# Kernel optimization log

Measured on AMD Instinct MI355X. Metric: run time of the kernel, lower is better.

## Reference

```python
import jax, jax.numpy as jnp
import numpy as np

D = 256; HEADS = 8; DH = D // HEADS; LEVELS = 4; POINTS = 4; NLAYERS = 6; DFF = 1024
SHAPES = ((92, 160), (46, 80), (23, 40), (12, 20))  # (H, W) per level
LEN = sum(h * w for h, w in SHAPES)  # 19560
BS = 4; NQ = 900; EPS = 1e-5
SCALE = 1.0 / float(np.sqrt(DH))


def setup_inputs() -> dict:
    ks = iter(jax.random.split(jax.random.key(0), 64))
    def rn(shape, s=0.02):
        return jax.random.normal(next(ks), shape, jnp.float32) * s
    inp = {}
    inp['tgt'] = jax.random.normal(next(ks), (BS, NQ, D), jnp.float32)
    inp['reference_points'] = jax.random.uniform(next(ks), (BS, NQ, 3), jnp.float32)
    inp['src'] = jax.random.normal(next(ks), (BS, LEN, D), jnp.float32)
    inp['valid_ratios'] = jnp.ones((BS, LEVELS, 2), jnp.float32)
    inp['query_pos'] = jax.random.normal(next(ks), (BS, NQ, D), jnp.float32)
    # per-layer stacked parameters [NLAYERS, ...]
    inp['sa_in_w'] = rn((NLAYERS, 3 * D, D)); inp['sa_in_b'] = jnp.zeros((NLAYERS, 3 * D))
    inp['sa_out_w'] = rn((NLAYERS, D, D)); inp['sa_out_b'] = jnp.zeros((NLAYERS, D))
    inp['samp_w'] = rn((NLAYERS, HEADS * LEVELS * POINTS * 2, D), 0.01)
    inp['samp_b'] = jax.random.uniform(next(ks), (NLAYERS, HEADS * LEVELS * POINTS * 2), jnp.float32, -2.0, 2.0)
    inp['attn_w'] = rn((NLAYERS, HEADS * LEVELS * POINTS, D)); inp['attn_b'] = jnp.zeros((NLAYERS, HEADS * LEVELS * POINTS))
    inp['val_w'] = rn((NLAYERS, D, D)); inp['val_b'] = jnp.zeros((NLAYERS, D))
    inp['ca_out_w'] = rn((NLAYERS, D, D)); inp['ca_out_b'] = jnp.zeros((NLAYERS, D))
    inp['ffn1_w'] = rn((NLAYERS, DFF, D)); inp['ffn1_b'] = jnp.zeros((NLAYERS, DFF))
    inp['ffn2_w'] = rn((NLAYERS, D, DFF)); inp['ffn2_b'] = jnp.zeros((NLAYERS, D))
    for i in (1, 2, 3):
        inp['ln%d_w' % i] = jnp.ones((NLAYERS, D)); inp['ln%d_b' % i] = jnp.zeros((NLAYERS, D))
    return inp


def _ln(x, w, b):
    mu = x.mean(-1, keepdims=True)
    var = ((x - mu) ** 2).mean(-1, keepdims=True)
    return (x - mu) / jnp.sqrt(var + EPS) * w + b


def _self_attn(q, k, v, in_w, in_b, out_w, out_b):
    wq, wk, wv = jnp.split(in_w, 3, 0)
    bq, bk, bv = jnp.split(in_b, 3, 0)
    def proj(x, w, b):
        return (x @ w.T + b).reshape(BS, -1, HEADS, DH).transpose(0, 2, 1, 3)
    qh, kh, vh = proj(q, wq, bq), proj(k, wk, bk), proj(v, wv, bv)
    att = jax.nn.softmax(jnp.einsum('bhqd,bhkd->bhqk', qh * SCALE, kh), axis=-1)
    o = jnp.einsum('bhqk,bhkd->bhqd', att, vh).transpose(0, 2, 1, 3).reshape(BS, -1, D)
    return o @ out_w.T + out_b


def _msda(query, ref, src, sw, sb, aw, ab, vw, vb, ow, ob):
    # query [bs,NQ,D]; ref [bs,NQ,LEVELS,2] normalized xz coords
    value = (src @ vw.T + vb).reshape(BS, LEN, HEADS, DH)
    off = (query @ sw.T + sb).reshape(BS, NQ, HEADS, LEVELS, POINTS, 2)
    attn = jax.nn.softmax((query @ aw.T + ab).reshape(BS, NQ, HEADS, LEVELS * POINTS), -1)
    attn = attn.reshape(BS, NQ, HEADS, LEVELS, POINTS)
    norm = jnp.asarray([[w, h] for h, w in SHAPES], jnp.float32)  # (W,H) per level
    loc = ref[:, :, None, :, None, :] + off / norm[None, None, None, :, None, :]
    out = jnp.zeros((BS, HEADS, NQ, DH), jnp.float32)
    start = 0
    for l, (H, W) in enumerate(SHAPES):
        v_l = value[:, start:start + H * W].transpose(0, 2, 1, 3)  # [bs,heads,HW,dh]
        start += H * W
        ll = loc[:, :, :, l]  # [bs,NQ,heads,P,2]
        x = ll[..., 0] * W - 0.5
        y = ll[..., 1] * H - 0.5
        x0 = jnp.floor(x); y0 = jnp.floor(y)
        fx = x - x0; fy = y - y0
        x0i = x0.astype(jnp.int32); y0i = y0.astype(jnp.int32)
        def gather(xi, yi):
            inb = ((xi >= 0) & (xi < W) & (yi >= 0) & (yi < H)).astype(jnp.float32)
            idx = jnp.clip(yi, 0, H - 1) * W + jnp.clip(xi, 0, W - 1)
            idxt = idx.transpose(0, 2, 1, 3).reshape(BS, HEADS, NQ * POINTS, 1)
            g = jnp.take_along_axis(v_l, idxt, axis=2).reshape(BS, HEADS, NQ, POINTS, DH)
            return g * inb.transpose(0, 2, 1, 3)[..., None]
        def wt(w4):
            return w4.transpose(0, 2, 1, 3)[..., None]
        samp = (gather(x0i, y0i) * wt((1 - fx) * (1 - fy))
                + gather(x0i + 1, y0i) * wt(fx * (1 - fy))
                + gather(x0i, y0i + 1) * wt((1 - fx) * fy)
                + gather(x0i + 1, y0i + 1) * wt(fx * fy))
        out = out + (samp * attn[:, :, :, l].transpose(0, 2, 1, 3)[..., None]).sum(3)
    out = out.transpose(0, 2, 1, 3).reshape(BS, NQ, D)
    return out @ ow.T + ob


def _forward(tgt, reference_points, src, valid_ratios, query_pos,
             sa_in_w, sa_in_b, sa_out_w, sa_out_b,
             samp_w, samp_b, attn_w, attn_b, val_w, val_b, ca_out_w, ca_out_b,
             ffn1_w, ffn1_b, ffn2_w, ffn2_b,
             ln1_w, ln1_b, ln2_w, ln2_b, ln3_w, ln3_b):
    # reference_points last dim == 3 (x,y,z); deformable attn uses (x,z)
    ref_xz = jnp.concatenate([reference_points[..., :1], reference_points[..., 2:]], -1)
    ref_in = ref_xz[:, :, None] * valid_ratios[:, None]  # [bs,NQ,LEVELS,2]
    out = tgt
    for l in range(NLAYERS):
        q = out + query_pos
        sa = _self_attn(q, q, out, sa_in_w[l], sa_in_b[l], sa_out_w[l], sa_out_b[l])
        out = _ln(out + sa, ln1_w[l], ln1_b[l])
        ca = _msda(out + query_pos, ref_in, src, samp_w[l], samp_b[l], attn_w[l], attn_b[l],
                   val_w[l], val_b[l], ca_out_w[l], ca_out_b[l])
        out = _ln(out + ca, ln2_w[l], ln2_b[l])
        h = jax.nn.relu(out @ ffn1_w[l].T + ffn1_b[l]) @ ffn2_w[l].T + ffn2_b[l]
        out = _ln(out + h, ln3_w[l], ln3_b[l])
    return out


def reference(tgt, reference_points, src, valid_ratios, query_pos,
              sa_in_w, sa_in_b, sa_out_w, sa_out_b,
              samp_w, samp_b, attn_w, attn_b, val_w, val_b, ca_out_w, ca_out_b,
              ffn1_w, ffn1_b, ffn2_w, ffn2_b,
              ln1_w, ln1_b, ln2_w, ln2_b, ln3_w, ln3_b):
    return _forward(tgt, reference_points, src, valid_ratios, query_pos,
                    sa_in_w, sa_in_b, sa_out_w, sa_out_b,
                    samp_w, samp_b, attn_w, attn_b, val_w, val_b, ca_out_w, ca_out_b,
                    ffn1_w, ffn1_b, ffn2_w, ffn2_b,
                    ln1_w, ln1_b, ln2_w, ln2_b, ln3_w, ln3_b)
```

## Files before the change

### kernel.cpp

```cpp
#include <hip/hip_runtime.h>
#include <math.h>

#define DMODEL 256
#define HEADS 8
#define DHEAD 32
#define LEVELS 4
#define POINTS 4
#define NLAYERS 6
#define DFF 1024
#define BS 4
#define NQ 900
#define SLEN 19560
#define EPS_LN 1e-5f
#define ATT_SCALE 0.17677669529663689f

typedef __attribute__((ext_vector_type(8))) short bf16x8;
typedef __attribute__((ext_vector_type(4))) float f32x4;
typedef __attribute__((ext_vector_type(4))) unsigned short u16x4;
typedef __attribute__((ext_vector_type(8))) unsigned short u16x8;

__device__ __forceinline__ unsigned short f2b(float x) {
  unsigned u = __float_as_uint(x);
  u += 0x7FFF + ((u >> 16) & 1);
  return (unsigned short)(u >> 16);
}
__device__ __forceinline__ float b2f(unsigned short v) {
  return __uint_as_float(((unsigned)v) << 16);
}

__global__ __launch_bounds__(256) void copycvt_k(const float* __restrict__ a,
                                                 const float* __restrict__ qp,
                                                 float* __restrict__ cf,
                                                 unsigned short* __restrict__ cb,
                                                 unsigned short* __restrict__ qb, int n4) {
  int i = blockIdx.x * 256 + threadIdx.x;
  if (i < n4) {
    float4 v = reinterpret_cast<const float4*>(a)[i];
    float4 q = reinterpret_cast<const float4*>(qp)[i];
    reinterpret_cast<float4*>(cf)[i] = v;
    u16x4 o4 = {f2b(v.x), f2b(v.y), f2b(v.z), f2b(v.w)};
    reinterpret_cast<u16x4*>(cb)[i] = o4;
    u16x4 p4 = {f2b(v.x + q.x), f2b(v.y + q.y), f2b(v.z + q.z), f2b(v.w + q.w)};
    reinterpret_cast<u16x4*>(qb)[i] = p4;
  }
}

#define N4_SRC (SLEN * BS * DMODEL / 4)
#define N4_SAIN (NLAYERS * 768 * 256 / 4)
#define N4_SQ (NLAYERS * 256 * 256 / 4)
#define N4_FFN (NLAYERS * DFF * 256 / 4)
__global__ __launch_bounds__(256) void f2ball_k(
    const float* __restrict__ s0, const float* __restrict__ s1,
    const float* __restrict__ s2, const float* __restrict__ s3,
    const float* __restrict__ s4, const float* __restrict__ s5,
    const float* __restrict__ s6,
    unsigned short* __restrict__ d0, unsigned short* __restrict__ d1,
    unsigned short* __restrict__ d2, unsigned short* __restrict__ d3,
    unsigned short* __restrict__ d4, unsigned short* __restrict__ d5,
    unsigned short* __restrict__ d6) {
  const int total = N4_SRC + N4_SAIN + 3 * N4_SQ + 2 * N4_FFN;
  for (int i = blockIdx.x * 256 + threadIdx.x; i < total; i += gridDim.x * 256) {
    const float* s;
    unsigned short* d;
    int j = i;
    if (j < N4_SRC) { s = s0; d = d0; }
    else { j -= N4_SRC;
      if (j < N4_SAIN) { s = s1; d = d1; }
      else { j -= N4_SAIN;
        if (j < N4_SQ) { s = s2; d = d2; }
        else { j -= N4_SQ;
          if (j < N4_SQ) { s = s3; d = d3; }
          else { j -= N4_SQ;
            if (j < N4_SQ) { s = s4; d = d4; }
            else { j -= N4_SQ;
              if (j < N4_FFN) { s = s5; d = d5; }
              else { j -= N4_FFN; s = s6; d = d6; } } } } } }
    float4 v = reinterpret_cast<const float4*>(s)[j];
    u16x4 o4 = {f2b(v.x), f2b(v.y), f2b(v.z), f2b(v.w)};
    reinterpret_cast<u16x4*>(d)[j] = o4;
  }
}

__global__ __launch_bounds__(256) void catw_k(const float* __restrict__ sw,
                                              const float* __restrict__ aw,
                                              const float* __restrict__ sb,
                                              const float* __restrict__ ab,
                                              unsigned short* __restrict__ wout,
                                              float* __restrict__ bout) {
  int i = blockIdx.x * 256 + threadIdx.x;
  const int total4 = NLAYERS * 384 * 256 / 4;
  if (i < total4) {
    int l = i / (384 * 64);
    int r = i % (384 * 64);
    int row = r / 64;
    int c4 = r % 64;
    const float* srcp = row < 256
        ? sw + ((size_t)l * 256 * 256 + (size_t)row * 256 + c4 * 4)
        : aw + ((size_t)l * 128 * 256 + (size_t)(row - 256) * 256 + c4 * 4);
    float4 v = *(const float4*)srcp;
    u16x4 o4 = {f2b(v.x), f2b(v.y), f2b(v.z), f2b(v.w)};
    *(u16x4*)(wout + (size_t)i * 4) = o4;
  }
  if (i < NLAYERS * 384) {
    int l = i / 384, r = i % 384;
    bout[i] = r < 256 ? sb[l * 256 + r] : ab[l * 128 + (r - 256)];
  }
}

__global__ __launch_bounds__(256) void gemm_bf_k(const unsigned short* __restrict__ A,
                                                 const unsigned short* __restrict__ W,
                                                 const float* __restrict__ bias,
                                                 const float* __restrict__ res,
                                                 float* __restrict__ outf,
                                                 unsigned short* __restrict__ outb,
                                                 int ldo, int M, int N, int K, int relu) {
  __shared__ unsigned short As[64][72];
  __shared__ unsigned short Ws[64][72];
  const int tid = threadIdx.x;
  const int lane = tid & 63, wv = tid >> 6;
  const int wm = wv >> 1, wn = wv & 1;
  const int m0 = blockIdx.x * 64, n0 = blockIdx.y * 64;
  const int l15 = lane & 15, l4 = lane >> 4;

  f32x4 acc[2][2] = {};
  for (int k0 = 0; k0 < K; k0 += 64) {
#pragma unroll
    for (int t = 0; t < 2; ++t) {
      int u = t * 256 + tid;
      int r = u >> 3, c8 = u & 7;
      int ra = m0 + r; if (ra >= M) ra = M - 1;
      *(u16x8*)&As[r][c8 * 8] = *(const u16x8*)(A + (size_t)ra * K + k0 + c8 * 8);
      *(u16x8*)&Ws[r][c8 * 8] = *(const u16x8*)(W + (size_t)(n0 + r) * K + k0 + c8 * 8);
    }
    __syncthreads();
#pragma unroll
    for (int ks = 0; ks < 64; ks += 32) {
      bf16x8 af[2], wf[2];
#pragma unroll
      for (int fr = 0; fr < 2; ++fr)
        af[fr] = *(const bf16x8*)&As[wm * 32 + fr * 16 + l15][ks + l4 * 8];
#pragma unroll
      for (int fn = 0; fn < 2; ++fn)
        wf[fn] = *(const bf16x8*)&Ws[wn * 32 + fn * 16 + l15][ks + l4 * 8];
#pragma unroll
      for (int fr = 0; fr < 2; ++fr)
#pragma unroll
        for (int fn = 0; fn < 2; ++fn)
          acc[fr][fn] = __builtin_amdgcn_mfma_f32_16x16x32_bf16(
              af[fr], wf[fn], acc[fr][fn], 0, 0, 0);
    }
    __syncthreads();
  }
#pragma unroll
  for (int fr = 0; fr < 2; ++fr)
#pragma unroll
    for (int fn = 0; fn < 2; ++fn) {
      int col = n0 + wn * 32 + fn * 16 + l15;
      float bs = bias[col];
#pragma unroll
      for (int j = 0; j < 4; ++j) {
        int row = m0 + wm * 32 + fr * 16 + l4 * 4 + j;
        if (row >= M) continue;
        float v = acc[fr][fn][j] + bs;
        if (res) v += res[(size_t)row * ldo + col];
        if (relu) v = fmaxf(v, 0.f);
        if (outf) outf[(size_t)row * ldo + col] = v;
        if (outb) outb[(size_t)row * ldo + col] = f2b(v);
      }
    }
}

__global__ __launch_bounds__(256) void gemm_vmfma_k(const unsigned short* __restrict__ A,
                                                    const unsigned short* __restrict__ W,
                                                    const float* __restrict__ bias,
                                                    unsigned short* __restrict__ C,
                                                    int M) {
  __shared__ unsigned short As[128][72];
  __shared__ unsigned short Ws[128][72];
  const int tid = threadIdx.x;
  const int lane = tid & 63, wv = tid >> 6;
  const int wm = wv >> 1, wn = wv & 1;
  const int m0 = blockIdx.x * 128, n0 = blockIdx.y * 128;
  const int l15 = lane & 15, l4 = lane >> 4;

  f32x4 acc[4][4] = {};

  for (int k0 = 0; k0 < 256; k0 += 64) {
#pragma unroll
    for (int t = 0; t < 4; ++t) {
      int u = t * 256 + tid;
      int r = u >> 3, c8 = u & 7;
      int ra = m0 + r; if (ra >= M) ra = M - 1;
      *(u16x8*)&As[r][c8 * 8] = *(const u16x8*)(A + (size_t)ra * 256 + k0 + c8 * 8);
      *(u16x8*)&Ws[r][c8 * 8] = *(const u16x8*)(W + (size_t)(n0 + r) * 256 + k0 + c8 * 8);
    }
    __syncthreads();
#pragma unroll
    for (int ks = 0; ks < 64; ks += 32) {
      bf16x8 af[4], bf[4];
#pragma unroll
      for (int fr = 0; fr < 4; ++fr)
        af[fr] = *(const bf16x8*)&As[wm * 64 + fr * 16 + l15][ks + l4 * 8];
#pragma unroll
      for (int fn = 0; fn < 4; ++fn)
        bf[fn] = *(const bf16x8*)&Ws[wn * 64 + fn * 16 + l15][ks + l4 * 8];
#pragma unroll
      for (int fr = 0; fr < 4; ++fr)
#pragma unroll
        for (int fn = 0; fn < 4; ++fn)
          acc[fr][fn] = __builtin_amdgcn_mfma_f32_16x16x32_bf16(
              af[fr], bf[fn], acc[fr][fn], 0, 0, 0);
    }
    __syncthreads();
  }
#pragma unroll
  for (int fr = 0; fr < 4; ++fr)
#pragma unroll
    for (int fn = 0; fn < 4; ++fn) {
      int col = n0 + wn * 64 + fn * 16 + l15;
      float bs = bias[col];
#pragma unroll
      for (int j = 0; j < 4; ++j) {
        int row = m0 + wm * 64 + fr * 16 + l4 * 4 + j;
        if (row < M) C[(size_t)row * 256 + col] = f2b(acc[fr][fn][j] + bs);
      }
    }
}

__global__ __launch_bounds__(256) void fattn_mfma_k(const unsigned short* __restrict__ qkv,
                                                    unsigned short* __restrict__ o) {
  __shared__ unsigned short Qlds[64][40];
  __shared__ unsigned short Klds[64][40];
  __shared__ unsigned short Vt[32][72];
  __shared__ unsigned short Plds[64][72];
  const int tid = threadIdx.x;
  const int lane = tid & 63;
  const int wq = tid >> 6;
  const int l15 = lane & 15, l4 = lane >> 4;
  const int q0 = blockIdx.x * 64;
  const int h = blockIdx.y, b = blockIdx.z;
  const int hq = h * 32;
  const size_t rowb = (size_t)b * NQ;

  {
    int q = q0 + (tid >> 2);
    int qc = q < NQ ? q : NQ - 1;
    *(u16x8*)&Qlds[tid >> 2][(tid & 3) * 8] =
        *(const u16x8*)(qkv + (rowb + qc) * 768 + hq + (tid & 3) * 8);
  }
  __syncthreads();
  const bf16x8 qf = *(const bf16x8*)&Qlds[wq * 16 + l15][l4 * 8];

  float m_r[4] = {-1e30f, -1e30f, -1e30f, -1e30f};
  float l_r[4] = {0.f, 0.f, 0.f, 0.f};
  f32x4 oacc[2] = {};

  for (int k0 = 0; k0 < NQ; k0 += 64) {
    __syncthreads();
    {
      int kk = k0 + (tid >> 2);
      int kc = kk < NQ ? kk : NQ - 1;
      const unsigned short* kbase = qkv + (rowb + kc) * 768 + hq + (tid & 3) * 8;
      u16x8 kv = *(const u16x8*)(kbase + 256);
      u16x8 vv = *(const u16x8*)(kbase + 512);
      *(u16x8*)&Klds[tid >> 2][(tid & 3) * 8] = kv;
#pragma unroll
      for (int i = 0; i < 8; ++i) Vt[(tid & 3) * 8 + i][tid >> 2] = vv[i];
    }
    __syncthreads();

    f32x4 s[4];
#pragma unroll
    for (int fc = 0; fc < 4; ++fc) {
      bf16x8 kf = *(const bf16x8*)&Klds[fc * 16 + l15][l4 * 8];
      s[fc] = __builtin_amdgcn_mfma_f32_16x16x32_bf16(qf, kf, (f32x4){0.f, 0.f, 0.f, 0.f}, 0, 0, 0);
    }
#pragma unroll
    for (int fc = 0; fc < 4; ++fc) {
      bool oob = (k0 + fc * 16 + l15) >= NQ;
#pragma unroll
      for (int j = 0; j < 4; ++j)
        s[fc][j] = oob ? -1e30f : s[fc][j] * ATT_SCALE;
    }
#pragma unroll
    for (int j = 0; j < 4; ++j) {
      float tm = fmaxf(fmaxf(s[0][j], s[1][j]), fmaxf(s[2][j], s[3][j]));
      tm = fmaxf(tm, __shfl_xor(tm, 1, 16));
      tm = fmaxf(tm, __shfl_xor(tm, 2, 16));
      tm = fmaxf(tm, __shfl_xor(tm, 4, 16));
      tm = fmaxf(tm, __shfl_xor(tm, 8, 16));
      float mn = fmaxf(m_r[j], tm);
      float sf = __expf(m_r[j] - mn);
      m_r[j] = mn;
      oacc[0][j] *= sf;
      oacc[1][j] *= sf;
      float rs = 0.f;
#pragma unroll
      for (int fc = 0; fc < 4; ++fc) {
        float pv = __expf(s[fc][j] - mn);
        s[fc][j] = pv;
        rs += pv;
      }
      rs += __shfl_xor(rs, 1, 16);
      rs += __shfl_xor(rs, 2, 16);
      rs += __shfl_xor(rs, 4, 16);
      rs += __shfl_xor(rs, 8, 16);
      l_r[j] = l_r[j] * sf + rs;
    }
#pragma unroll
    for (int fc = 0; fc < 4; ++fc)
#pragma unroll
      for (int j = 0; j < 4; ++j)
        Plds[wq * 16 + l4 * 4 + j][fc * 16 + l15] = f2b(s[fc][j]);
    __syncthreads();
#pragma unroll
    for (int ks = 0; ks < 2; ++ks) {
      bf16x8 pf = *(const bf16x8*)&Plds[wq * 16 + l15][ks * 32 + l4 * 8];
#pragma unroll
      for (int oc = 0; oc < 2; ++oc) {
        bf16x8 vf = *(const bf16x8*)&Vt[oc * 16 + l15][ks * 32 + l4 * 8];
        oacc[oc] = __builtin_amdgcn_mfma_f32_16x16x32_bf16(pf, vf, oacc[oc], 0, 0, 0);
      }
    }
  }
#pragma unroll
  for (int j = 0; j < 4; ++j) {
    int q = q0 + wq * 16 + l4 * 4 + j;
    if (q < NQ) {
      float inv = 1.f / l_r[j];
      o[(rowb + q) * 256 + hq + l15] = f2b(oacc[0][j] * inv);
      o[(rowb + q) * 256 + hq + 16 + l15] = f2b(oacc[1][j] * inv);
    }
  }
}

__global__ __launch_bounds__(256) void msda_k(const float* __restrict__ refp,
                                              const float* __restrict__ vr,
                                              const unsigned short* __restrict__ value,
                                              const float* __restrict__ cat,
                                              unsigned short* __restrict__ outp) {
  const int HW[4][2] = {{92, 160}, {46, 80}, {23, 40}, {12, 20}};
  const int START[4] = {0, 14720, 18400, 19320};
  const int qi = blockIdx.x, b = blockIdx.y;
  const int tid = threadIdx.x;
  const int h = tid >> 5;
  const int r = tid & 31;
  const int lvl = r >> 3;
  const int li = r & 7;
  const size_t base = (size_t)(b * NQ + qi);
  const float rx = refp[base * 3 + 0];
  const float rz = refp[base * 3 + 2];

  const float* lg = cat + base * 384 + 256 + h * 16;
  float4 L0 = *(const float4*)(lg + 0);
  float4 L1 = *(const float4*)(lg + 4);
  float4 L2 = *(const float4*)(lg + 8);
  float4 L3 = *(const float4*)(lg + 12);
  float mx = fmaxf(fmaxf(fmaxf(L0.x, L0.y), fmaxf(L0.z, L0.w)),
                   fmaxf(fmaxf(fmaxf(L1.x, L1.y), fmaxf(L1.z, L1.w)),
                         fmaxf(fmaxf(fmaxf(L2.x, L2.y), fmaxf(L2.z, L2.w)),
                               fmaxf(fmaxf(L3.x, L3.y), fmaxf(L3.z, L3.w)))));
  float4 E0 = {__expf(L0.x - mx), __expf(L0.y - mx), __expf(L0.z - mx), __expf(L0.w - mx)};
  float4 E1 = {__expf(L1.x - mx), __expf(L1.y - mx), __expf(L1.z - mx), __expf(L1.w - mx)};
  float4 E2 = {__expf(L2.x - mx), __expf(L2.y - mx), __expf(L2.z - mx), __expf(L2.w - mx)};
  float4 E3 = {__expf(L3.x - mx), __expf(L3.y - mx), __expf(L3.z - mx), __expf(L3.w - mx)};
  float sum = E0.x + E0.y + E0.z + E0.w + E1.x + E1.y + E1.z + E1.w +
              E2.x + E2.y + E2.z + E2.w + E3.x + E3.y + E3.z + E3.w;
  const float inv = 1.f / sum;
  float4 Emy = lvl == 0 ? E0 : lvl == 1 ? E1 : lvl == 2 ? E2 : E3;
  float wl[4] = {Emy.x * inv, Emy.y * inv, Emy.z * inv, Emy.w * inv};

  const int H = HW[lvl][0], W = HW[lvl][1];
  const float refx = rx * vr[(b * LEVELS + lvl) * 2 + 0] * (float)W;
  const float refy = rz * vr[(b * LEVELS + lvl) * 2 + 1] * (float)H;
  const unsigned short* vbase = value + ((size_t)b * SLEN + START[lvl]) * DMODEL + h * DHEAD + li * 4;
  const float* ob = cat + base * 384 + h * 32 + lvl * 8;

  float a0 = 0.f, a1 = 0.f, a2 = 0.f, a3 = 0.f;
#pragma unroll
  for (int p = 0; p < 4; ++p) {
    const float x = refx + ob[p * 2 + 0] - 0.5f;
    const float y = refy + ob[p * 2 + 1] - 0.5f;
    const float x0f = floorf(x), y0f = floorf(y);
    const float fx = x - x0f, fy = y - y0f;
    const int x0 = (int)x0f, y0 = (int)y0f;
#pragma unroll
    for (int ci = 0; ci < 4; ++ci) {
      const int xi = x0 + (ci & 1);
      const int yi = y0 + (ci >> 1);
      if ((xi >= 0) && (xi < W) && (yi >= 0) && (yi < H)) {
        const float wxy = ((ci & 1) ? fx : 1.f - fx) * ((ci >> 1) ? fy : 1.f - fy) * wl[p];
        u16x4 v4 = *(const u16x4*)(vbase + (size_t)(yi * W + xi) * DMODEL);
        a0 = fmaf(wxy, b2f(v4[0]), a0);
        a1 = fmaf(wxy, b2f(v4[1]), a1);
        a2 = fmaf(wxy, b2f(v4[2]), a2);
        a3 = fmaf(wxy, b2f(v4[3]), a3);
      }
    }
  }
  a0 += __shfl_xor(a0, 8);  a1 += __shfl_xor(a1, 8);
  a2 += __shfl_xor(a2, 8);  a3 += __shfl_xor(a3, 8);
  a0 += __shfl_xor(a0, 16); a1 += __shfl_xor(a1, 16);
  a2 += __shfl_xor(a2, 16); a3 += __shfl_xor(a3, 16);
  if (lvl == 0) {
    u16x4 o4 = {f2b(a0), f2b(a1), f2b(a2), f2b(a3)};
    *(u16x4*)(outp + base * 256 + h * 32 + li * 4) = o4;
  }
}

__global__ __launch_bounds__(256) void ln_k(const float* __restrict__ src,
                                            const float* __restrict__ w,
                                            const float* __restrict__ bias,
                                            const float* __restrict__ qpos,
                                            float* __restrict__ dst,
                                            unsigned short* __restrict__ dstb,
                                            unsigned short* __restrict__ qposb) {
  const int row = blockIdx.x * 4 + (threadIdx.x >> 6);
  const int lane = threadIdx.x & 63;
  const size_t o = (size_t)row * DMODEL + lane * 4;
  float4 x = *(const float4*)(src + o);
  float s = x.x + x.y + x.z + x.w;
#pragma unroll
  for (int m = 1; m < 64; m <<= 1) s += __shfl_xor(s, m);
  const float mu = s * (1.f / DMODEL);
  float4 v = {x.x - mu, x.y - mu, x.z - mu, x.w - mu};
  float q = v.x * v.x + v.y * v.y + v.z * v.z + v.w * v.w;
#pragma unroll
  for (int m = 1; m < 64; m <<= 1) q += __shfl_xor(q, m);
  const float rstd = rsqrtf(q * (1.f / DMODEL) + EPS_LN);
  float4 wv = *(const float4*)(w + lane * 4);
  float4 bv = *(const float4*)(bias + lane * 4);
  float4 y = {v.x * rstd * wv.x + bv.x, v.y * rstd * wv.y + bv.y,
              v.z * rstd * wv.z + bv.z, v.w * rstd * wv.w + bv.w};
  *(float4*)(dst + o) = y;
  if (dstb) {
    u16x4 ob = {f2b(y.x), f2b(y.y), f2b(y.z), f2b(y.w)};
    *(u16x4*)(dstb + o) = ob;
  }
  if (qposb) {
    float4 qv = *(const float4*)(qpos + o);
    u16x4 ob = {f2b(y.x + qv.x), f2b(y.y + qv.y), f2b(y.z + qv.z), f2b(y.w + qv.w)};
    *(u16x4*)(qposb + o) = ob;
  }
}

extern "C" void kernel_launch(void* const* d_in, const int* in_sizes, int n_in,
                              void* d_out, int out_size, void* d_ws, size_t ws_size,
                              hipStream_t stream) {
  const float* tgt     = (const float*)d_in[0];
  const float* refp    = (const float*)d_in[1];
  const float* src     = (const float*)d_in[2];
  const float* vr      = (const float*)d_in[3];
  const float* qpos    = (const float*)d_in[4];
  const float* sa_in_w = (const float*)d_in[5];
  const float* sa_in_b = (const float*)d_in[6];
  const float* sa_out_w= (const float*)d_in[7];
  const float* sa_out_b= (const float*)d_in[8];
  const float* samp_w  = (const float*)d_in[9];
  const float* samp_b  = (const float*)d_in[10];
  const float* attn_w  = (const float*)d_in[11];
  const float* attn_b  = (const float*)d_in[12];
  const float* val_w   = (const float*)d_in[13];
  const float* val_b   = (const float*)d_in[14];
  const float* ca_out_w= (const float*)d_in[15];
  const float* ca_out_b= (const float*)d_in[16];
  const float* ffn1_w  = (const float*)d_in[17];
  const float* ffn1_b  = (const float*)d_in[18];
  const float* ffn2_w  = (const float*)d_in[19];
  const float* ffn2_b  = (const float*)d_in[20];
  const float* ln1_w   = (const float*)d_in[21];
  const float* ln1_b   = (const float*)d_in[22];
  const float* ln2_w   = (const float*)d_in[23];
  const float* ln2_b   = (const float*)d_in[24];
  const float* ln3_w   = (const float*)d_in[25];
  const float* ln3_b   = (const float*)d_in[26];

  const int M = BS * NQ;
  const int MV = BS * SLEN;
  const size_t TOK = (size_t)M * DMODEL;

  float* ws = (float*)d_ws;
  size_t off = 0;
  auto alloc = [&](size_t n) { float* p = ws + off; off += n; return p; };
  auto allocb = [&](size_t n) { unsigned short* p = (unsigned short*)(ws + off); off += (n + 1) / 2; return p; };
  float* cur    = alloc(TOK);
  float* tmp    = alloc(TOK);
  float* catout = alloc((size_t)M * 384);
  float* b_cacat= alloc((size_t)NLAYERS * 384);
  unsigned short* cur_bf  = allocb(TOK);
  unsigned short* qbuf_bf = allocb(TOK);
  unsigned short* sao_bf  = allocb(TOK);
  unsigned short* msda_bf = allocb(TOK);
  unsigned short* qkv_bf  = allocb((size_t)M * 768);
  unsigned short* ffnh_bf = allocb((size_t)M * DFF);
  unsigned short* src_bf  = allocb((size_t)MV * DMODEL);
  unsigned short* value_bf= allocb((size_t)MV * DMODEL);
  unsigned short* w_in_bf   = allocb((size_t)NLAYERS * 768 * 256);
  unsigned short* w_saout_bf= allocb((size_t)NLAYERS * 256 * 256);
  unsigned short* w_cacat_bf= allocb((size_t)NLAYERS * 384 * 256);
  unsigned short* w_val_bf  = allocb((size_t)NLAYERS * 256 * 256);
  unsigned short* w_caout_bf= allocb((size_t)NLAYERS * 256 * 256);
  unsigned short* w_ffn1_bf = allocb((size_t)NLAYERS * DFF * 256);
  unsigned short* w_ffn2_bf = allocb((size_t)NLAYERS * 256 * DFF);

  const int n4 = (int)(TOK / 4);
  const dim3 blk(256);
  const dim3 gE((n4 + 255) / 256);

  copycvt_k<<<gE, blk, 0, stream>>>(tgt, qpos, cur, cur_bf, qbuf_bf, n4);
  f2ball_k<<<dim3(2048), blk, 0, stream>>>(src, sa_in_w, sa_out_w, val_w, ca_out_w,
                                           ffn1_w, ffn2_w,
                                           src_bf, w_in_bf, w_saout_bf, w_val_bf,
                                           w_caout_bf, w_ffn1_bf, w_ffn2_bf);
  catw_k<<<dim3(576), blk, 0, stream>>>(samp_w, attn_w, samp_b, attn_b, w_cacat_bf, b_cacat);

  const dim3 gQK((M + 63) / 64, 512 / 64);
  const dim3 gV((M + 63) / 64, 256 / 64);
  const dim3 gN256((M + 63) / 64, 256 / 64);
  const dim3 gCat((M + 63) / 64, 384 / 64);
  const dim3 gF1((M + 63) / 64, DFF / 64);
  const dim3 gLN(M / 4);

  for (int l = 0; l < NLAYERS; ++l) {
    const unsigned short* wq = w_in_bf + (size_t)l * 768 * 256;
    const float* bq = sa_in_b + (size_t)l * 768;

    gemm_bf_k<<<gQK, blk, 0, stream>>>(qbuf_bf, wq, bq, nullptr,
                                       nullptr, qkv_bf, 768, M, 512, 256, 0);
    gemm_bf_k<<<gV, blk, 0, stream>>>(cur_bf, wq + 512 * 256, bq + 512, nullptr,
                                      nullptr, qkv_bf + 512, 768, M, 256, 256, 0);

    fattn_mfma_k<<<dim3((NQ + 63) / 64, HEADS, BS), blk, 0, stream>>>(qkv_bf, sao_bf);

    gemm_bf_k<<<gN256, blk, 0, stream>>>(sao_bf, w_saout_bf + (size_t)l * 256 * 256,
                                         sa_out_b + l * 256, cur, tmp, nullptr, 256, M, 256, 256, 0);
    ln_k<<<gLN, blk, 0, stream>>>(tmp, ln1_w + l * 256, ln1_b + l * 256, qpos,
                                  cur, nullptr, qbuf_bf);

    gemm_vmfma_k<<<dim3((MV + 127) / 128, 2), blk, 0, stream>>>(
        src_bf, w_val_bf + (size_t)l * 256 * 256, val_b + l * 256, value_bf, MV);
    gemm_bf_k<<<gCat, blk, 0, stream>>>(qbuf_bf, w_cacat_bf + (size_t)l * 384 * 256,
                                        b_cacat + l * 384, nullptr, catout, nullptr, 384, M, 384, 256, 0);

    msda_k<<<dim3(NQ, BS), blk, 0, stream>>>(refp, vr, value_bf, catout, msda_bf);

    gemm_bf_k<<<gN256, blk, 0, stream>>>(msda_bf, w_caout_bf + (size_t)l * 256 * 256,
                                         ca_out_b + l * 256, cur, tmp, nullptr, 256, M, 256, 256, 0);
    ln_k<<<gLN, blk, 0, stream>>>(tmp, ln2_w + l * 256, ln2_b + l * 256, nullptr,
                                  cur, cur_bf, nullptr);

    gemm_bf_k<<<gF1, blk, 0, stream>>>(cur_bf, w_ffn1_bf + (size_t)l * DFF * 256,
                                       ffn1_b + l * DFF, nullptr, nullptr, ffnh_bf, DFF, M, DFF, 256, 1);
    gemm_bf_k<<<gN256, blk, 0, stream>>>(ffnh_bf, w_ffn2_bf + (size_t)l * 256 * DFF,
                                         ffn2_b + l * 256, cur, tmp, nullptr, 256, M, 256, DFF, 0);
    const bool last = (l == NLAYERS - 1);
    ln_k<<<gLN, blk, 0, stream>>>(tmp, ln3_w + l * 256, ln3_b + l * 256,
                                  last ? nullptr : qpos,
                                  last ? (float*)d_out : cur,
                                  last ? nullptr : cur_bf,
                                  last ? nullptr : qbuf_bf);
  }
}
```

Measured before the change: 1.399 ms.

## Fuse residual+LayerNorm into GEMM epilogue and precompute query_pos projections

Adds a full-row GEMM kernel (32 rows x 256 cols per block) that applies bias, residual and LayerNorm in its epilogue, replacing the separate GEMM + ln_k pairs and the tmp buffer. Uses linearity to precompute query_pos projections for the Q/K and sampling/attention weights of all layers once up front. Per-layer GEMMs then take cur_bf as input and add the precomputed qpos term as a residual instead of bias, which also merges the QK and V projections into one launch. This trades extra workspace and one large upfront GEMM for fewer launches and fewer round trips through memory. The wide-N fused kernel has lower block-level parallelism and reloads the full 256-row weight tile per block.

```diff
diff --git a/kernel.cpp b/kernel.cpp
--- a/kernel.cpp
+++ b/kernel.cpp
@@ -40,7 +40,7 @@
     reinterpret_cast<float4*>(cf)[i] = v;
     u16x4 o4 = {f2b(v.x), f2b(v.y), f2b(v.z), f2b(v.w)};
     reinterpret_cast<u16x4*>(cb)[i] = o4;
-    u16x4 p4 = {f2b(v.x + q.x), f2b(v.y + q.y), f2b(v.z + q.z), f2b(v.w + q.w)};
+    u16x4 p4 = {f2b(q.x), f2b(q.y), f2b(q.z), f2b(q.w)};
     reinterpret_cast<u16x4*>(qb)[i] = p4;
   }
 }
@@ -107,10 +107,31 @@
   }
 }
 
+__global__ __launch_bounds__(256) void stackqk_k(const float* __restrict__ w_in,
+                                                 const float* __restrict__ b_in,
+                                                 unsigned short* __restrict__ qkW,
+                                                 float* __restrict__ bqk) {
+  int i = blockIdx.x * 256 + threadIdx.x;
+  const int total4 = NLAYERS * 512 * 256 / 4;
+  if (i < total4) {
+    int l = i / (512 * 64);
+    int r = i % (512 * 64);
+    int row = r / 64, c4 = r % 64;
+    float4 v = *(const float4*)(w_in + (size_t)l * 768 * 256 + (size_t)row * 256 + c4 * 4);
+    u16x4 o4 = {f2b(v.x), f2b(v.y), f2b(v.z), f2b(v.w)};
+    *(u16x4*)(qkW + ((size_t)(l * 512 + row) * 256 + c4 * 4)) = o4;
+  }
+  if (i < NLAYERS * 512) {
+    int l = i / 512, r = i % 512;
+    bqk[i] = b_in[l * 768 + r];
+  }
+}
+
 __global__ __launch_bounds__(256) void gemm_bf_k(const unsigned short* __restrict__ A,
                                                  const unsigned short* __restrict__ W,
                                                  const float* __restrict__ bias,
                                                  const float* __restrict__ res,
+                                                 int res_n, int ldr,
                                                  float* __restrict__ outf,
                                                  unsigned short* __restrict__ outb,
                                                  int ldo, int M, int N, int K, int relu) {
@@ -161,13 +182,106 @@
       for (int j = 0; j < 4; ++j) {
         int row = m0 + wm * 32 + fr * 16 + l4 * 4 + j;
         if (row >= M) continue;
-        float v = acc[fr][fn][j] + bs;
-        if (res) v += res[(size_t)row * ldo + col];
+        float v = acc[fr][fn][j];
+        if (res && col < res_n) v += res[(size_t)row * ldr + col];
+        else v += bs;
         if (relu) v = fmaxf(v, 0.f);
         if (outf) outf[(size_t)row * ldo + col] = v;
         if (outb) outb[(size_t)row * ldo + col] = f2b(v);
       }
     }
+}
+
+__global__ __launch_bounds__(256) void gemm_lnres_k(const unsigned short* __restrict__ A,
+                                                    const unsigned short* __restrict__ W,
+                                                    const float* __restrict__ bias,
+                                                    const float* __restrict__ res,
+                                                    const float* __restrict__ lnw,
+                                                    const float* __restrict__ lnb,
+                                                    float* __restrict__ outf,
+                                                    unsigned short* __restrict__ outb,
+                                                    int M, int K) {
+  __shared__ unsigned short As[32][72];
+  __shared__ unsigned short Ws[256][72];
+  __shared__ float Os[32][264];
+  const int tid = threadIdx.x;
+  const int lane = tid & 63, wv = tid >> 6;
+  const int l15 = lane & 15, l4 = lane >> 4;
+  const int m0 = blockIdx.x * 32;
+
+  f32x4 acc[2][4] = {};
+  for (int k0 = 0; k0 < K; k0 += 64) {
+    {
+      int r = tid >> 3, c8 = tid & 7;
+      int ra = m0 + r; if (ra >= M) ra = M - 1;
+      *(u16x8*)&As[r][c8 * 8] = *(const u16x8*)(A + (size_t)ra * K + k0 + c8 * 8);
+#pragma unroll
+      for (int t = 0; t < 8; ++t) {
+        int u = t * 256 + tid;
+        int wr = u >> 3, wc = u & 7;
+        *(u16x8*)&Ws[wr][wc * 8] = *(const u16x8*)(W + (size_t)wr * K + k0 + wc * 8);
+      }
+    }
+    __syncthreads();
+#pragma unroll
+    for (int ks = 0; ks < 64; ks += 32) {
+      bf16x8 af[2], wf[4];
+#pragma unroll
+      for (int fr = 0; fr < 2; ++fr)
+        af[fr] = *(const bf16x8*)&As[fr * 16 + l15][ks + l4 * 8];
+#pragma unroll
+      for (int fc = 0; fc < 4; ++fc)
+        wf[fc] = *(const bf16x8*)&Ws[wv * 64 + fc * 16 + l15][ks + l4 * 8];
+#pragma unroll
+      for (int fr = 0; fr < 2; ++fr)
+#pragma unroll
+        for (int fc = 0; fc < 4; ++fc)
+          acc[fr][fc] = __builtin_amdgcn_mfma_f32_16x16x32_bf16(
+              af[fr], wf[fc], acc[fr][fc], 0, 0, 0);
+    }
+    __syncthreads();
+  }
+#pragma unroll
+  for (int fr = 0; fr < 2; ++fr)
+#pragma unroll
+    for (int fc = 0; fc < 4; ++fc) {
+      int col = wv * 64 + fc * 16 + l15;
+      float bs = bias[col];
+#pragma unroll
+      for (int j = 0; j < 4; ++j) {
+        int row = fr * 16 + l4 * 4 + j;
+        int grow = m0 + row;
+        float v = acc[fr][fc][j] + bs + (grow < M ? res[(size_t)grow * 256 + col] : 0.f);
+        Os[row][col] = v;
+      }
+    }
+  __syncthreads();
+  float4 wv4 = *(const float4*)(lnw + lane * 4);
+  float4 bv4 = *(const float4*)(lnb + lane * 4);
+#pragma unroll
+  for (int i = 0; i < 8; ++i) {
+    int row = wv * 8 + i;
+    int grow = m0 + row;
+    float4 x = *(float4*)&Os[row][lane * 4];
+    float s = x.x + x.y + x.z + x.w;
+#pragma unroll
+    for (int m = 1; m < 64; m <<= 1) s += __shfl_xor(s, m);
+    const float mu = s * (1.f / DMODEL);
+    float4 v = {x.x - mu, x.y - mu, x.z - mu, x.w - mu};
+    float q = v.x * v.x + v.y * v.y + v.z * v.z + v.w * v.w;
+#pragma unroll
+    for (int m = 1; m < 64; m <<= 1) q += __shfl_xor(q, m);
+    const float rstd = rsqrtf(q * (1.f / DMODEL) + EPS_LN);
+    float4 y = {v.x * rstd * wv4.x + bv4.x, v.y * rstd * wv4.y + bv4.y,
+                v.z * rstd * wv4.z + bv4.z, v.w * rstd * wv4.w + bv4.w};
+    if (grow < M) {
+      *(float4*)(outf + (size_t)grow * 256 + lane * 4) = y;
+      if (outb) {
+        u16x4 ob = {f2b(y.x), f2b(y.y), f2b(y.z), f2b(y.w)};
+        *(u16x4*)(outb + (size_t)grow * 256 + lane * 4) = ob;
+      }
+    }
+  }
 }
 
 __global__ __launch_bounds__(256) void gemm_vmfma_k(const unsigned short* __restrict__ A,
@@ -405,42 +519,6 @@
   if (lvl == 0) {
     u16x4 o4 = {f2b(a0), f2b(a1), f2b(a2), f2b(a3)};
     *(u16x4*)(outp + base * 256 + h * 32 + li * 4) = o4;
-  }
-}
-
-__global__ __launch_bounds__(256) void ln_k(const float* __restrict__ src,
-                                            const float* __restrict__ w,
-                                            const float* __restrict__ bias,
-                                            const float* __restrict__ qpos,
-                                            float* __restrict__ dst,
-                                            unsigned short* __restrict__ dstb,
-                                            unsigned short* __restrict__ qposb) {
-  const int row = blockIdx.x * 4 + (threadIdx.x >> 6);
-  const int lane = threadIdx.x & 63;
-  const size_t o = (size_t)row * DMODEL + lane * 4;
-  float4 x = *(const float4*)(src + o);
-  float s = x.x + x.y + x.z + x.w;
-#pragma unroll
-  for (int m = 1; m < 64; m <<= 1) s += __shfl_xor(s, m);
-  const float mu = s * (1.f / DMODEL);
-  float4 v = {x.x - mu, x.y - mu, x.z - mu, x.w - mu};
-  float q = v.x * v.x + v.y * v.y + v.z * v.z + v.w * v.w;
-#pragma unroll
-  for (int m = 1; m < 64; m <<= 1) q += __shfl_xor(q, m);
-  const float rstd = rsqrtf(q * (1.f / DMODEL) + EPS_LN);
-  float4 wv = *(const float4*)(w + lane * 4);
-  float4 bv = *(const float4*)(bias + lane * 4);
-  float4 y = {v.x * rstd * wv.x + bv.x, v.y * rstd * wv.y + bv.y,
-              v.z * rstd * wv.z + bv.z, v.w * rstd * wv.w + bv.w};
-  *(float4*)(dst + o) = y;
-  if (dstb) {
-    u16x4 ob = {f2b(y.x), f2b(y.y), f2b(y.z), f2b(y.w)};
-    *(u16x4*)(dstb + o) = ob;
-  }
-  if (qposb) {
-    float4 qv = *(const float4*)(qpos + o);
-    u16x4 ob = {f2b(y.x + qv.x), f2b(y.y + qv.y), f2b(y.z + qv.z), f2b(y.w + qv.w)};
-    *(u16x4*)(qposb + o) = ob;
   }
 }
 
@@ -483,12 +561,14 @@
   size_t off = 0;
   auto alloc = [&](size_t n) { float* p = ws + off; off += n; return p; };
   auto allocb = [&](size_t n) { unsigned short* p = (unsigned short*)(ws + off); off += (n + 1) / 2; return p; };
-  float* cur    = alloc(TOK);
-  float* tmp    = alloc(TOK);
-  float* catout = alloc((size_t)M * 384);
-  float* b_cacat= alloc((size_t)NLAYERS * 384);
+  float* cur     = alloc(TOK);
+  float* catout  = alloc((size_t)M * 384);
+  float* b_cacat = alloc((size_t)NLAYERS * 384);
+  float* bqk     = alloc((size_t)NLAYERS * 512);
+  float* qpos_qk = alloc((size_t)M * NLAYERS * 512);
+  float* qpos_cat= alloc((size_t)M * NLAYERS * 384);
   unsigned short* cur_bf  = allocb(TOK);
-  unsigned short* qbuf_bf = allocb(TOK);
+  unsigned short* qpos_bf = allocb(TOK);
   unsigned short* sao_bf  = allocb(TOK);
   unsigned short* msda_bf = allocb(TOK);
   unsigned short* qkv_bf  = allocb((size_t)M * 768);
@@ -502,62 +582,64 @@
   unsigned short* w_caout_bf= allocb((size_t)NLAYERS * 256 * 256);
   unsigned short* w_ffn1_bf = allocb((size_t)NLAYERS * DFF * 256);
   unsigned short* w_ffn2_bf = allocb((size_t)NLAYERS * 256 * DFF);
+  unsigned short* qkW_bf    = allocb((size_t)NLAYERS * 512 * 256);
 
   const int n4 = (int)(TOK / 4);
   const dim3 blk(256);
   const dim3 gE((n4 + 255) / 256);
 
-  copycvt_k<<<gE, blk, 0, stream>>>(tgt, qpos, cur, cur_bf, qbuf_bf, n4);
+  copycvt_k<<<gE, blk, 0, stream>>>(tgt, qpos, cur, cur_bf, qpos_bf, n4);
   f2ball_k<<<dim3(2048), blk, 0, stream>>>(src, sa_in_w, sa_out_w, val_w, ca_out_w,
                                            ffn1_w, ffn2_w,
                                            src_bf, w_in_bf, w_saout_bf, w_val_bf,
                                            w_caout_bf, w_ffn1_bf, w_ffn2_bf);
   catw_k<<<dim3(576), blk, 0, stream>>>(samp_w, attn_w, samp_b, attn_b, w_cacat_bf, b_cacat);
-
-  const dim3 gQK((M + 63) / 64, 512 / 64);
-  const dim3 gV((M + 63) / 64, 256 / 64);
-  const dim3 gN256((M + 63) / 64, 256 / 64);
-  const dim3 gCat((M + 63) / 64, 384 / 64);
-  const dim3 gF1((M + 63) / 64, DFF / 64);
-  const dim3 gLN(M / 4);
+  stackqk_k<<<dim3(768), blk, 0, stream>>>(sa_in_w, sa_in_b, qkW_bf, bqk);
+  gemm_bf_k<<<dim3(57, 48), blk, 0, stream>>>(qpos_bf, qkW_bf, bqk, nullptr, 0, 0,
+                                              qpos_qk, nullptr, 3072, M, 3072, 256, 0);
+  gemm_bf_k<<<dim3(57, 36), blk, 0, stream>>>(qpos_bf, w_cacat_bf, b_cacat, nullptr, 0, 0,
+                                              qpos_cat, nullptr, 2304, M, 2304, 256, 0);
+
+  const dim3 gQKV(57, 12);
+  const dim3 gCat(57, 6);
+  const dim3 gF1(57, 16);
+  const dim3 gLN(113);
 
   for (int l = 0; l < NLAYERS; ++l) {
-    const unsigned short* wq = w_in_bf + (size_t)l * 768 * 256;
-    const float* bq = sa_in_b + (size_t)l * 768;
-
-    gemm_bf_k<<<gQK, blk, 0, stream>>>(qbuf_bf, wq, bq, nullptr,
-                                       nullptr, qkv_bf, 768, M, 512, 256, 0);
-    gemm_bf_k<<<gV, blk, 0, stream>>>(cur_bf, wq + 512 * 256, bq + 512, nullptr,
-                                      nullptr, qkv_bf + 512, 768, M, 256, 256, 0);
+    gemm_bf_k<<<gQKV, blk, 0, stream>>>(cur_bf, w_in_bf + (size_t)l * 768 * 256,
+                                        sa_in_b + l * 768,
+                                        qpos_qk + (size_t)l * 512, 512, 3072,
+                                        nullptr, qkv_bf, 768, M, 768, 256, 0);
 
     fattn_mfma_k<<<dim3((NQ + 63) / 64, HEADS, BS), blk, 0, stream>>>(qkv_bf, sao_bf);
 
-    gemm_bf_k<<<gN256, blk, 0, stream>>>(sao_bf, w_saout_bf + (size_t)l * 256 * 256,
-                                         sa_out_b + l * 256, cur, tmp, nullptr, 256, M, 256, 256, 0);
-    ln_k<<<gLN, blk, 0, stream>>>(tmp, ln1_w + l * 256, ln1_b + l * 256, qpos,
-                                  cur, nullptr, qbuf_bf);
+    gemm_lnres_k<<<gLN, blk, 0, stream>>>(sao_bf, w_saout_bf + (size_t)l * 256 * 256,
+                                          sa_out_b + l * 256, cur,
+                                          ln1_w + l * 256, ln1_b + l * 256,
+                                          cur, cur_bf, M, 256);
 
     gemm_vmfma_k<<<dim3((MV + 127) / 128, 2), blk, 0, stream>>>(
         src_bf, w_val_bf + (size_t)l * 256 * 256, val_b + l * 256, value_bf, MV);
-    gemm_bf_k<<<gCat, blk, 0, stream>>>(qbuf_bf, w_cacat_bf + (size_t)l * 384 * 256,
-                                        b_cacat + l * 384, nullptr, catout, nullptr, 384, M, 384, 256, 0);
+    gemm_bf_k<<<gCat, blk, 0, stream>>>(cur_bf, w_cacat_bf + (size_t)l * 384 * 256,
+                                        b_cacat + l * 384,
+                                        qpos_cat + (size_t)l * 384, 384, 2304,
+                                        catout, nullptr, 384, M, 384, 256, 0);
 
     msda_k<<<dim3(NQ, BS), blk, 0, stream>>>(refp, vr, value_bf, catout, msda_bf);
 
-    gemm_bf_k<<<gN256, blk, 0, stream>>>(msda_bf, w_caout_bf + (size_t)l * 256 * 256,
-                                         ca_out_b + l * 256, cur, tmp, nullptr, 256, M, 256, 256, 0);
-    ln_k<<<gLN, blk, 0, stream>>>(tmp, ln2_w + l * 256, ln2_b + l * 256, nullptr,
-                                  cur, cur_bf, nullptr);
+    gemm_lnres_k<<<gLN, blk, 0, stream>>>(msda_bf, w_caout_bf + (size_t)l * 256 * 256,
+                                          ca_out_b + l * 256, cur,
+                                          ln2_w + l * 256, ln2_b + l * 256,
+                                          cur, cur_bf, M, 256);
 
     gemm_bf_k<<<gF1, blk, 0, stream>>>(cur_bf, w_ffn1_bf + (size_t)l * DFF * 256,
-                                       ffn1_b + l * DFF, nullptr, nullptr, ffnh_bf, DFF, M, DFF, 256, 1);
-    gemm_bf_k<<<gN256, blk, 0, stream>>>(ffnh_bf, w_ffn2_bf + (size_t)l * 256 * DFF,
-                                         ffn2_b + l * 256, cur, tmp, nullptr, 256, M, 256, DFF, 0);
+                                       ffn1_b + l * DFF, nullptr, 0, 0,
+                                       nullptr, ffnh_bf, DFF, M, DFF, 256, 1);
     const bool last = (l == NLAYERS - 1);
-    ln_k<<<gLN, blk, 0, stream>>>(tmp, ln3_w + l * 256, ln3_b + l * 256,
-                                  last ? nullptr : qpos,
-                                  last ? (float*)d_out : cur,
-                                  last ? nullptr : cur_bf,
-                                  last ? nullptr : qbuf_bf);
-  }
-}
+    gemm_lnres_k<<<gLN, blk, 0, stream>>>(ffnh_bf, w_ffn2_bf + (size_t)l * 256 * DFF,
+                                          ffn2_b + l * 256, cur,
+                                          ln3_w + l * 256, ln3_b + l * 256,
+                                          last ? (float*)d_out : cur,
+                                          last ? nullptr : cur_bf, M, DFF);
+  }
+}
```

Result: no change. 1.407 ms (+0.5%).
